# Kernel tuning notes

Measured on AMD Instinct MI355X. Metric: run time of the kernel, lower is better.

The kernel has to match this reference:

```python
import jax, jax.numpy as jnp
import numpy as np

N, E, D_IN, HID, HEADS, TS_OUT = 100000, 200000, 165, 64, 8, 5
HD1 = HID // HEADS  # 8 per-head channels in layer 1
HD2 = HID           # 64 per-head channels in layer 2 (concat=False -> mean)


def _glorot(key, shape):
    fan_in, fan_out = shape[0], shape[1]
    s = np.sqrt(6.0 / (fan_in + fan_out)).astype(np.float32)
    return jax.random.uniform(key, shape, jnp.float32, -s, s)


def setup_inputs() -> dict:
    key = jax.random.key(0)
    ks = jax.random.split(key, 24)
    inp = {
        "x": jax.random.normal(ks[0], (N, D_IN), jnp.float32),
        "edge_index": jax.random.randint(ks[1], (2, E), 0, N, jnp.int32),
        "timestamp_target": jax.random.randint(ks[2], (N,), 0, TS_OUT, jnp.int32),
        "node_target": jax.random.randint(ks[3], (N,), 0, 2, jnp.int32),
        "node_mask": jax.random.randint(ks[4], (N,), 0, 2, jnp.int32).astype(jnp.bool_),
        # GATConv layer 1: in=165 -> 8 heads x 8 ch, concat -> 64
        "W1": _glorot(ks[5], (D_IN, HEADS * HD1)),
        "att_src1": _glorot(ks[6], (HEADS, HD1)),
        "att_dst1": _glorot(ks[7], (HEADS, HD1)),
        "b1": jnp.zeros((HEADS * HD1,), jnp.float32),
        # GATConv layer 2: in=64 -> 8 heads x 64 ch, mean -> 64
        "W2": _glorot(ks[8], (HID, HEADS * HD2)),
        "att_src2": _glorot(ks[9], (HEADS, HD2)),
        "att_dst2": _glorot(ks[10], (HEADS, HD2)),
        "b2": jnp.zeros((HD2,), jnp.float32),
        # timestamp predictor MLP
        "ts_w1": _glorot(ks[11], (HID, HID)), "ts_b1": jnp.zeros((HID,), jnp.float32),
        "ts_w2": _glorot(ks[12], (HID, TS_OUT)), "ts_b2": jnp.zeros((TS_OUT,), jnp.float32),
        # class predictor MLP
        "cls_w1": _glorot(ks[13], (HID, HID)), "cls_b1": jnp.zeros((HID,), jnp.float32),
        "cls_w2": _glorot(ks[14], (HID, 2)), "cls_b2": jnp.zeros((2,), jnp.float32),
    }
    return inp


def _gat_layer(x, src, dst, n, W, a_src, a_dst, b, concat):
    H, C = a_src.shape
    h = (x @ W).reshape(n, H, C)                      # [N,H,C]
    a_s = (h * a_src).sum(-1)                         # [N,H]
    a_d = (h * a_dst).sum(-1)                         # [N,H]
    alpha = jax.nn.leaky_relu(a_s[src] + a_d[dst], 0.2)   # [E,H]
    amax = jax.ops.segment_max(alpha, dst, num_segments=n)
    ea = jnp.exp(alpha - amax[dst])
    denom = jax.ops.segment_sum(ea, dst, num_segments=n)
    a = ea / (denom[dst] + 1e-16)                     # segment softmax over incoming edges
    out = jax.ops.segment_sum(h[src] * a[:, :, None], dst, num_segments=n)  # [N,H,C]
    out = out.reshape(n, H * C) if concat else out.mean(axis=1)
    return out + b


def _ce(logits, targets):
    lp = jax.nn.log_softmax(logits, axis=-1)
    return -jnp.take_along_axis(lp, targets[:, None].astype(jnp.int32), axis=1)[:, 0]


def reference(x, edge_index, timestamp_target, node_target, node_mask,
              W1, att_src1, att_dst1, b1, W2, att_src2, att_dst2, b2,
              ts_w1, ts_b1, ts_w2, ts_b2, cls_w1, cls_b1, cls_w2, cls_b2):
    n = x.shape[0]
    loops = jnp.arange(n, dtype=edge_index.dtype)
    src = jnp.concatenate([edge_index[0], loops])     # add self loops (PyG default)
    dst = jnp.concatenate([edge_index[1], loops])
    h = _gat_layer(x, src, dst, n, W1, att_src1, att_dst1, b1, True)   # [N,64]
    h = _gat_layer(h, src, dst, n, W2, att_src2, att_dst2, b2, False)  # [N,64]
    # gradient reversal is identity in the forward pass
    ts_pred = jax.nn.relu(h @ ts_w1 + ts_b1) @ ts_w2 + ts_b2           # [N,5]
    cls_pred = jax.nn.relu(h @ cls_w1 + cls_b1) @ cls_w2 + cls_b2      # [N,2]
    ts_loss = _ce(ts_pred, timestamp_target).mean()
    m = node_mask.astype(jnp.float32)
    cls_loss = (_ce(cls_pred, node_target) * m).sum() / m.sum()
    return cls_loss + 1.0 * ts_loss
```

## Files before the change

kernel.cpp:

```cpp
#include <hip/hip_runtime.h>
#include <hip/hip_bf16.h>

#define NN 100000
#define NE 200000
#define NT (NE + NN)
#define DIN 165
#define CHUNK 50000
#define PREPB 128
#define INITB 391
#define PACKB 8
#define W1PB 24
#define MISCGRID (PREPB + INITB + PACKB + W1PB)
#define NODEB 1563
#define XDW ((size_t)NN * DIN)
#define NDMA 42

typedef __attribute__((ext_vector_type(8))) short bf16x8_t;
typedef __attribute__((ext_vector_type(4))) float f32x4_t;
typedef _Float16 h2_t __attribute__((ext_vector_type(2)));
typedef _Float16 f16x8_t __attribute__((ext_vector_type(8)));

#define AS1 __attribute__((address_space(1)))
#define AS3 __attribute__((address_space(3)))

static __device__ __forceinline__ unsigned short f2bf(float f) {
    __hip_bfloat16 b = __float2bfloat16(f);
    return *(unsigned short*)&b;
}
static __device__ __forceinline__ float bfu(unsigned short u) {
    __hip_bfloat16 b = *(__hip_bfloat16*)&u;
    return __bfloat162float(b);
}
static __device__ __forceinline__ unsigned pkh2(float a, float b) {
    h2_t v; v[0] = (_Float16)a; v[1] = (_Float16)b;
    return *(unsigned*)&v;
}


__global__ __launch_bounds__(256) void k_misc(const float* W2, const float* a2s, const float* a2d,
                                              float* wsd, __hip_bfloat16* W2pT,
                                              int* cnt, int* fill,
                                              const float* tsw1, const float* cw1,
                                              unsigned* tswp, unsigned* cwp,
                                              const float* W1, unsigned* W1pT, float* zbuf) {
    int b = blockIdx.x;
    int tid = threadIdx.x;
    if (b < PREPB) {
        int i = b * 256 + tid;
        int c = i >> 9, j = i & 511;
        int hh = j >> 6, kk = j & 63;
        W2pT[i] = __float2bfloat16(W2[kk * 512 + hh * 64 + c]);
        if (b == 0) zbuf[tid] = 0.f;
        if (i < 512) {
            int h = i >> 6, k = i & 63;
            float s = 0.f, d = 0.f;
            for (int cc = 0; cc < 64; cc++) {
                float w = W2[k * 512 + h * 64 + cc];
                s += w * a2s[h * 64 + cc];
                d += w * a2d[h * 64 + cc];
            }
            wsd[i] = s; wsd[512 + i] = d;
        }
    } else if (b < PREPB + INITB) {
        int i = (b - PREPB) * 256 + tid;
        if (i < NN) { cnt[i] = 0; fill[i] = 0; }
    } else if (b < PREPB + INITB + PACKB) {
        int i = (b - PREPB - INITB) * 256 + tid;
        if (i < 2048) {
            int kp = i >> 6, c = i & 63;
            tswp[i] = pkh2(tsw1[(2 * kp) * 64 + c], tsw1[(2 * kp + 1) * 64 + c]);
            cwp[i]  = pkh2(cw1[(2 * kp) * 64 + c],  cw1[(2 * kp + 1) * 64 + c]);
        }
    } else {
        int i = (b - PREPB - INITB - PACKB) * 256 + tid;
        if (i < 6144) {
            int c = i / 96, kp = i - c * 96;
            int k = 2 * kp;
            float f0 = (k < DIN) ? W1[k * 64 + c] : 0.f;
            float f1 = (k + 1 < DIN) ? W1[(k + 1) * 64 + c] : 0.f;
            W1pT[i] = pkh2(f0, f1);
        }
    }
}


__global__ __launch_bounds__(256) void k_count(const int* dstE, int* cnt) {
    int e = blockIdx.x * 256 + threadIdx.x;
    if (e < NE) atomicAdd(&cnt[dstE[e]], 1);
}

__global__ __launch_bounds__(256) void k_scanA(const int* cnt, int* rowptr, int* bsum) {
    __shared__ int sm[256];
    int t = threadIdx.x;
    int base = blockIdx.x * 1024;
    int v[4]; int s = 0;
    for (int i = 0; i < 4; i++) {
        int idx = base + t * 4 + i;
        v[i] = (idx < NN) ? (cnt[idx] + 1) : 0;
        s += v[i];
    }
    sm[t] = s; __syncthreads();
    for (int off = 1; off < 256; off <<= 1) {
        int x = (t >= off) ? sm[t - off] : 0;
        __syncthreads();
        sm[t] += x;
        __syncthreads();
    }
    int run = sm[t] - s;
    for (int i = 0; i < 4; i++) {
        run += v[i];
        int idx = base + t * 4 + i;
        if (idx < NN) rowptr[idx + 1] = run;
    }
    if (t == 255) bsum[blockIdx.x] = sm[255];
}

__global__ __launch_bounds__(64) void k_scanB(int* bsum, int nb) {
    int lane = threadIdx.x;
    int v0 = (lane < nb) ? bsum[lane] : 0;
    int v1 = (64 + lane < nb) ? bsum[64 + lane] : 0;
    int s0 = v0;
    for (int off = 1; off < 64; off <<= 1) { int t = __shfl_up(s0, off); if (lane >= off) s0 += t; }
    int tot0 = __shfl(s0, 63);
    int s1 = v1;
    for (int off = 1; off < 64; off <<= 1) { int t = __shfl_up(s1, off); if (lane >= off) s1 += t; }
    if (lane < nb) bsum[lane] = s0 - v0;
    if (64 + lane < nb) bsum[64 + lane] = tot0 + s1 - v1;
}

__global__ __launch_bounds__(256) void k_scanC(const int* bsum, int* rowptr) {
    int i = blockIdx.x * 256 + threadIdx.x;
    if (i < NN) rowptr[i + 1] += bsum[i >> 10];
    if (i == 0) rowptr[0] = 0;
}

__global__ __launch_bounds__(256) void k_fill(const int* srcE, const int* dstE,
                                              const int* rowptr, int* fill, int* col, int* rowv) {
    int i = blockIdx.x * 256 + threadIdx.x;
    if (i >= NT) return;
    int s, d;
    if (i < NE) { s = srcE[i]; d = dstE[i]; }
    else        { s = i - NE; d = s; }
    int p = rowptr[d] + atomicAdd(&fill[d], 1);
    col[p] = s;
    rowv[p] = d;
}


__global__ __launch_bounds__(256) void k_gemm1(const float* x, const unsigned* W1pT,
                                               const float* att_s, const float* att_d,
                                               const float* zsrc,
                                               __hip_bfloat16* h1b, float* aad1) {
    __shared__ float X[NDMA * 256];
    int tid = threadIdx.x;
    int l = tid & 63, w = tid >> 6;
    int n0 = blockIdx.x * 64;
    int frow = l & 15, kg = l >> 4;

    size_t tb = (size_t)n0 * DIN;
    for (int i = w; i < NDMA; i += 4) {
        size_t gd = tb + (size_t)i * 256 + (size_t)l * 4;
        const float* g = (gd + 4 <= XDW) ? (x + gd) : (zsrc + l * 4);
        __builtin_amdgcn_global_load_lds((const AS1 float*)g,
                                         (AS3 float*)(X + i * 256), 16, 0, 0);
    }
    uint4 B[6][4];
    #pragma unroll
    for (int s = 0; s < 6; s++)
        #pragma unroll
        for (int t = 0; t < 4; t++)
            B[s][t] = *(const uint4*)&W1pT[(t * 16 + frow) * 96 + s * 16 + kg * 4];
    __syncthreads();

    f32x4_t acc[4] = {};
    int rbase = (w * 16 + frow) * DIN + kg * 8;
    #pragma unroll
    for (int s = 0; s < 6; s++) {
        float f[8];
        #pragma unroll
        for (int j = 0; j < 8; j++) f[j] = X[rbase + s * 32 + j];
        f16x8_t av;
        #pragma unroll
        for (int j = 0; j < 8; j++) av[j] = (_Float16)f[j];
        #pragma unroll
        for (int t = 0; t < 4; t++)
            acc[t] = __builtin_amdgcn_mfma_f32_16x16x32_f16(av, *(f16x8_t*)&B[s][t], acc[t], 0, 0, 0);
    }

    int nw = n0 + w * 16;
    float asv[4], adv[4];
    #pragma unroll
    for (int t = 0; t < 4; t++) {
        int c = t * 16 + frow;
        asv[t] = att_s[c]; adv[t] = att_d[c];
    }
    int hb = (l >> 3) & 1;
    #pragma unroll
    for (int q = 0; q < 4; q++) {
        int n = nw + kg * 4 + q;
        bool ok = (n < NN);
        #pragma unroll
        for (int t = 0; t < 4; t++) {
            float sv = acc[t][q] * asv[t];
            float dv = acc[t][q] * adv[t];
            sv += __shfl_xor(sv, 1); sv += __shfl_xor(sv, 2); sv += __shfl_xor(sv, 4);
            dv += __shfl_xor(dv, 1); dv += __shfl_xor(dv, 2); dv += __shfl_xor(dv, 4);
            if (ok && (l & 7) == 0) {
                int h = t * 2 + hb;
                aad1[(size_t)n * 16 + h]     = sv;
                aad1[(size_t)n * 16 + 8 + h] = dv;
            }
        }
    }

    __syncthreads();
    unsigned short* Hw = (unsigned short*)X + w * 1152;
    #pragma unroll
    for (int t = 0; t < 4; t++)
        #pragma unroll
        for (int q = 0; q < 4; q++)
            Hw[(kg * 4 + q) * 72 + t * 16 + frow] = f2bf(acc[t][q]);
    int rr = l >> 2, cc = l & 3;
    int n2 = nw + rr;
    if (n2 < NN) {
        unsigned short* dst = (unsigned short*)h1b + (size_t)n2 * 64 + cc * 16;
        *(uint4*)dst       = *(const uint4*)&Hw[rr * 72 + cc * 16];
        *(uint4*)(dst + 8) = *(const uint4*)&Hw[rr * 72 + cc * 16 + 8];
    }
}


__global__ __launch_bounds__(256) void k_edgew(const float* aad, const int* col, const int* rowv,
                                               __hip_bfloat16* web) {
    int e = blockIdx.x * 256 + threadIdx.x;
    if (e >= NT) return;
    int s = col[e], d = rowv[e];
    float4 s0 = *(const float4*)&aad[(size_t)s * 16];
    float4 s1 = *(const float4*)&aad[(size_t)s * 16 + 4];
    float4 dd0 = *(const float4*)&aad[(size_t)d * 16 + 8];
    float4 dd1 = *(const float4*)&aad[(size_t)d * 16 + 12];
    float as[8] = {s0.x, s0.y, s0.z, s0.w, s1.x, s1.y, s1.z, s1.w};
    float ad[8] = {dd0.x, dd0.y, dd0.z, dd0.w, dd1.x, dd1.y, dd1.z, dd1.w};
    unsigned p[4];
    #pragma unroll
    for (int q = 0; q < 4; q++) {
        float a0 = as[2*q]   + ad[2*q];
        float a1 = as[2*q+1] + ad[2*q+1];
        a0 = a0 > 0.f ? a0 : 0.2f * a0;
        a1 = a1 > 0.f ? a1 : 0.2f * a1;
        p[q] = (unsigned)f2bf(__expf(a0)) | ((unsigned)f2bf(__expf(a1)) << 16);
    }
    *(uint4*)&web[(size_t)e * 8] = make_uint4(p[0], p[1], p[2], p[3]);
}


__global__ __launch_bounds__(256) void k_agg1(const __hip_bfloat16* h1b, const __hip_bfloat16* we1b,
                                              const int* rowptr, const int* col,
                                              const float* b1, __hip_bfloat16* out1b) {
    int tid = threadIdx.x;
    int q = tid & 15;
    int n = blockIdx.x * 16 + (tid >> 4);
    int hq = q >> 1;
    const unsigned short* h1u = (const unsigned short*)h1b;
    const unsigned short* weu = (const unsigned short*)we1b;
    int rs = rowptr[n], re = rowptr[n + 1];
    float acc0 = 0.f, acc1 = 0.f, acc2 = 0.f, acc3 = 0.f, den = 0.f;
    for (int eb = rs; eb < re; eb += 4) {
        int c4[4];
        #pragma unroll
        for (int j = 0; j < 4; j++) c4[j] = col[min(eb + j, re - 1)];
        #pragma unroll
        for (int j = 0; j < 4; j++) {
            int e = min(eb + j, re - 1);
            float wv = bfu(weu[(size_t)e * 8 + hq]);
            wv = (eb + j < re) ? wv : 0.f;
            uint2 hv = *(const uint2*)&h1u[(size_t)c4[j] * 64 + q * 4];
            den  += wv;
            acc0 += wv * bfu((unsigned short)(hv.x & 0xffff));
            acc1 += wv * bfu((unsigned short)(hv.x >> 16));
            acc2 += wv * bfu((unsigned short)(hv.y & 0xffff));
            acc3 += wv * bfu((unsigned short)(hv.y >> 16));
        }
    }
    float4 bb = *(const float4*)&b1[q * 4];
    float dd = den + 1e-16f;
    unsigned short* ou = (unsigned short*)out1b;
    unsigned p0 = (unsigned)f2bf(acc0 / dd + bb.x) | ((unsigned)f2bf(acc1 / dd + bb.y) << 16);
    unsigned p1 = (unsigned)f2bf(acc2 / dd + bb.z) | ((unsigned)f2bf(acc3 / dd + bb.w) << 16);
    *(uint2*)&ou[(size_t)n * 64 + q * 4] = make_uint2(p0, p1);
}


__global__ __launch_bounds__(256) void k_att2(const __hip_bfloat16* out1b, const float* wsd,
                                              float* aad2) {
    __shared__ float t[64][65];
    int tid = threadIdx.x;
    int n0 = blockIdx.x * 64;
    const unsigned short* o1u = (const unsigned short*)out1b;
    #pragma unroll
    for (int l = 0; l < 4; l++) {
        int q = tid + l * 256;
        int r = q >> 4, c4 = q & 15;
        int n = n0 + r;
        uint2 v = make_uint2(0, 0);
        if (n < NN) v = *(const uint2*)&o1u[(size_t)n * 64 + c4 * 4];
        t[r][c4 * 4 + 0] = bfu((unsigned short)(v.x & 0xffff));
        t[r][c4 * 4 + 1] = bfu((unsigned short)(v.x >> 16));
        t[r][c4 * 4 + 2] = bfu((unsigned short)(v.y & 0xffff));
        t[r][c4 * 4 + 3] = bfu((unsigned short)(v.y >> 16));
    }
    __syncthreads();
    int lane = tid & 63;
    int j0 = __builtin_amdgcn_readfirstlane((tid >> 6) * 4);
    int n = n0 + lane;
    float a0 = 0.f, a1 = 0.f, a2 = 0.f, a3 = 0.f;
    #pragma unroll 8
    for (int k = 0; k < 64; k++) {
        float ov = t[lane][k];
        a0 += ov * wsd[(j0 + 0) * 64 + k];
        a1 += ov * wsd[(j0 + 1) * 64 + k];
        a2 += ov * wsd[(j0 + 2) * 64 + k];
        a3 += ov * wsd[(j0 + 3) * 64 + k];
    }
    if (n < NN) *(float4*)&aad2[(size_t)n * 16 + j0] = make_float4(a0, a1, a2, a3);
}


__global__ __launch_bounds__(256) void k_agg2(const __hip_bfloat16* out1b, const __hip_bfloat16* we2b,
                                              const int* rowptr, const int* col,
                                              __hip_bfloat16* aggb, int n0, int n1) {
    int tid = threadIdx.x;
    int p = tid & 31;
    int n = n0 + blockIdx.x * 8 + (tid >> 5);
    const unsigned short* o1u = (const unsigned short*)out1b;
    const unsigned short* weu = (const unsigned short*)we2b;
    int rs = rowptr[n], re = rowptr[n + 1];
    float den[8] = {}, a0[8] = {}, a1[8] = {};
    for (int eb = rs; eb < re; eb += 4) {
        int c4[4];
        #pragma unroll
        for (int j = 0; j < 4; j++) c4[j] = col[min(eb + j, re - 1)];
        #pragma unroll
        for (int j = 0; j < 4; j++) {
            int e = min(eb + j, re - 1);
            uint4 wv = *(const uint4*)&weu[(size_t)e * 8];
            unsigned hv = *(const unsigned*)&o1u[(size_t)c4[j] * 64 + p * 2];
            float vmul = (eb + j < re) ? 1.f : 0.f;
            float h0 = bfu((unsigned short)(hv & 0xffff));
            float h1 = bfu((unsigned short)(hv >> 16));
            float wts[8] = {bfu((unsigned short)(wv.x & 0xffff)), bfu((unsigned short)(wv.x >> 16)),
                            bfu((unsigned short)(wv.y & 0xffff)), bfu((unsigned short)(wv.y >> 16)),
                            bfu((unsigned short)(wv.z & 0xffff)), bfu((unsigned short)(wv.z >> 16)),
                            bfu((unsigned short)(wv.w & 0xffff)), bfu((unsigned short)(wv.w >> 16))};
            #pragma unroll
            for (int hh = 0; hh < 8; hh++) {
                float ww = wts[hh] * vmul;
                den[hh] += ww;
                a0[hh] += ww * h0;
                a1[hh] += ww * h1;
            }
        }
    }
    size_t base = (size_t)(n - n0) * 512;
    unsigned short* au = (unsigned short*)aggb;
    #pragma unroll
    for (int hh = 0; hh < 8; hh++) {
        float dd = den[hh] + 1e-16f;
        unsigned pp = (unsigned)f2bf(a0[hh] / dd) | ((unsigned)f2bf(a1[hh] / dd) << 16);
        *(unsigned*)&au[base + hh * 64 + p * 2] = pp;
    }
}


__global__ __launch_bounds__(256) void k_gemm2(const __hip_bfloat16* aggb, const __hip_bfloat16* W2pT,
                                               const float* b2, __hip_bfloat16* out2Tb, int n0, int n1) {
    __shared__ float smem[4608];
    unsigned short* A_lds = (unsigned short*)smem;
    unsigned short* B_lds = A_lds + 64 * 72;
    const unsigned short* A_g = (const unsigned short*)aggb;
    const unsigned short* B_g = (const unsigned short*)W2pT;
    int tid = threadIdx.x;
    int w = tid >> 6, l = tid & 63;
    int m0 = blockIdx.x * 64;
    int rows = n1 - n0;
    f32x4_t acc[4] = {};
    for (int k0 = 0; k0 < 512; k0 += 64) {
        #pragma unroll
        for (int ll = 0; ll < 2; ll++) {
            int u = tid + ll * 256;
            int r = u >> 3, seg = u & 7;
            uint4 va = make_uint4(0, 0, 0, 0);
            if (m0 + r < rows) va = *(const uint4*)&A_g[(size_t)(m0 + r) * 512 + k0 + seg * 8];
            *(uint4*)&A_lds[r * 72 + seg * 8] = va;
            *(uint4*)&B_lds[r * 72 + seg * 8] = *(const uint4*)&B_g[(size_t)r * 512 + k0 + seg * 8];
        }
        __syncthreads();
        #pragma unroll
        for (int kk = 0; kk < 2; kk++) {
            bf16x8_t a = *(const bf16x8_t*)&A_lds[(w * 16 + (l & 15)) * 72 + kk * 32 + (l >> 4) * 8];
            #pragma unroll
            for (int t = 0; t < 4; t++) {
                bf16x8_t bb = *(const bf16x8_t*)&B_lds[(t * 16 + (l & 15)) * 72 + kk * 32 + (l >> 4) * 8];
                acc[t] = __builtin_amdgcn_mfma_f32_16x16x32_bf16(a, bb, acc[t], 0, 0, 0);
            }
        }
        __syncthreads();
    }
    #pragma unroll
    for (int t = 0; t < 4; t++) {
        int col_l = l & 15;
        float bias = b2[t * 16 + col_l];
        #pragma unroll
        for (int q = 0; q < 4; q++) {
            int row_l = (l >> 4) * 4 + q;
            smem[(w * 16 + row_l) * 66 + t * 16 + col_l] = 0.125f * acc[t][q] + bias;
        }
    }
    __syncthreads();
    unsigned short* o2u = (unsigned short*)out2Tb;
    int ml = tid & 63, cr = tid >> 6;
    #pragma unroll
    for (int p = 0; p < 16; p++) {
        int c = p * 4 + cr;
        int gr = m0 + ml;
        if (gr < rows) o2u[(size_t)c * NN + (n0 + gr)] = f2bf(smem[ml * 66 + c]);
    }
}


__global__ __launch_bounds__(256) void k_mlp(const __hip_bfloat16* out2Tb,
                                             const unsigned* tswp, const float* tsb1,
                                             const float* tsw2, const float* tsb2,
                                             const unsigned* cwp, const float* cb1,
                                             const float* cw2, const float* cb2,
                                             const int* tst, const int* ctg, const unsigned char* msk,
                                             float* part) {
    __shared__ unsigned t2h[32 * 64];
    __shared__ float red[4][7][64];
    int tid = threadIdx.x;
    int lane = tid & 63;
    int w = tid >> 6;
    int n0 = blockIdx.x * 64;
    int nstage = n0 + lane; if (nstage >= NN) nstage = NN - 1;
    const unsigned short* o2u = (const unsigned short*)out2Tb;
    #pragma unroll
    for (int l = 0; l < 8; l++) {
        int kp = w * 8 + l;
        float e0 = bfu(o2u[(size_t)(2 * kp) * NN + nstage]);
        float e1 = bfu(o2u[(size_t)(2 * kp + 1) * NN + nstage]);
        t2h[kp * 64 + lane] = pkh2(e0, e1);
    }
    __syncthreads();

    int c0 = __builtin_amdgcn_readfirstlane(w * 16);
    int n = n0 + lane;
    float vts[16], vcls[16];
    #pragma unroll
    for (int j = 0; j < 16; j++) { vts[j] = tsb1[c0 + j]; vcls[j] = cb1[c0 + j]; }
    for (int kp = 0; kp < 32; kp++) {
        unsigned ou = t2h[kp * 64 + lane];
        h2_t ov = *(h2_t*)&ou;
        const unsigned* wt = &tswp[kp * 64 + c0];
        const unsigned* wc = &cwp[kp * 64 + c0];
        #pragma unroll
        for (int j = 0; j < 16; j++) {
            unsigned wtv = wt[j], wcv = wc[j];
            vts[j]  = __builtin_amdgcn_fdot2(ov, *(h2_t*)&wtv, vts[j], false);
            vcls[j] = __builtin_amdgcn_fdot2(ov, *(h2_t*)&wcv, vcls[j], false);
        }
    }
    float lg[5] = {0.f, 0.f, 0.f, 0.f, 0.f};
    float lg2[2] = {0.f, 0.f};
    #pragma unroll
    for (int j = 0; j < 16; j++) {
        int c = c0 + j;
        float v = fmaxf(vts[j], 0.f);
        #pragma unroll
        for (int t = 0; t < 5; t++) lg[t] += v * tsw2[c * 5 + t];
        float v2 = fmaxf(vcls[j], 0.f);
        lg2[0] += v2 * cw2[c * 2];
        lg2[1] += v2 * cw2[c * 2 + 1];
    }
    #pragma unroll
    for (int t = 0; t < 5; t++) red[w][t][lane] = lg[t];
    red[w][5][lane] = lg2[0];
    red[w][6][lane] = lg2[1];
    __syncthreads();
    if (w == 0) {
        float tsl = 0.f, cll = 0.f, mval = 0.f;
        if (n < NN) {
            float L[5];
            #pragma unroll
            for (int t = 0; t < 5; t++)
                L[t] = red[0][t][lane] + red[1][t][lane] + red[2][t][lane] + red[3][t][lane] + tsb2[t];
            float mx = L[0];
            #pragma unroll
            for (int t = 1; t < 5; t++) mx = fmaxf(mx, L[t]);
            float se = 0.f;
            #pragma unroll
            for (int t = 0; t < 5; t++) se += __expf(L[t] - mx);
            int tg = tst[n];
            float pick = 0.f;
            #pragma unroll
            for (int t = 0; t < 5; t++) pick += (t == tg) ? L[t] : 0.f;
            tsl = mx + __logf(se) - pick;
            float C0 = red[0][5][lane] + red[1][5][lane] + red[2][5][lane] + red[3][5][lane] + cb2[0];
            float C1 = red[0][6][lane] + red[1][6][lane] + red[2][6][lane] + red[3][6][lane] + cb2[1];
            float mx2 = fmaxf(C0, C1);
            float lse2 = mx2 + __logf(__expf(C0 - mx2) + __expf(C1 - mx2));
            mval = msk[n] ? 1.f : 0.f;
            float pick2 = ctg[n] ? C1 : C0;
            cll = (lse2 - pick2) * mval;
        }
        #pragma unroll
        for (int off = 1; off < 64; off <<= 1) {
            tsl  += __shfl_xor(tsl, off);
            cll  += __shfl_xor(cll, off);
            mval += __shfl_xor(mval, off);
        }
        if (lane == 0) {
            part[blockIdx.x * 3 + 0] = tsl;
            part[blockIdx.x * 3 + 1] = cll;
            part[blockIdx.x * 3 + 2] = mval;
        }
    }
}

__global__ __launch_bounds__(256) void k_final(const float* part, float* out, int nb) {
    __shared__ float sm[3][256];
    int tid = threadIdx.x;
    float a = 0, b = 0, c = 0;
    for (int i = tid; i < nb; i += 256) { a += part[i*3]; b += part[i*3+1]; c += part[i*3+2]; }
    sm[0][tid] = a; sm[1][tid] = b; sm[2][tid] = c;
    __syncthreads();
    for (int s = 128; s > 0; s >>= 1) {
        if (tid < s) {
            sm[0][tid] += sm[0][tid + s];
            sm[1][tid] += sm[1][tid + s];
            sm[2][tid] += sm[2][tid + s];
        }
        __syncthreads();
    }
    if (tid == 0) out[0] = sm[1][0] / sm[2][0] + sm[0][0] / (float)NN;
}


extern "C" void kernel_launch(void* const* d_in, const int* in_sizes, int n_in,
                              void* d_out, int out_size, void* d_ws, size_t ws_size,
                              hipStream_t stream) {
    const float* x    = (const float*)d_in[0];
    const int*   ei   = (const int*)d_in[1];
    const int*   tst  = (const int*)d_in[2];
    const int*   ctg  = (const int*)d_in[3];
    const unsigned char* msk = (const unsigned char*)d_in[4];
    const float* W1   = (const float*)d_in[5];
    const float* a1s  = (const float*)d_in[6];
    const float* a1d  = (const float*)d_in[7];
    const float* b1   = (const float*)d_in[8];
    const float* W2   = (const float*)d_in[9];
    const float* a2s  = (const float*)d_in[10];
    const float* a2d  = (const float*)d_in[11];
    const float* b2   = (const float*)d_in[12];
    const float* tsw1 = (const float*)d_in[13];
    const float* tsb1 = (const float*)d_in[14];
    const float* tsw2 = (const float*)d_in[15];
    const float* tsb2 = (const float*)d_in[16];
    const float* cw1  = (const float*)d_in[17];
    const float* cb1  = (const float*)d_in[18];
    const float* cw2  = (const float*)d_in[19];
    const float* cb2  = (const float*)d_in[20];
    const int* srcE = ei;
    const int* dstE = ei + NE;

    char* ws = (char*)d_ws;
    size_t off = 0;
    auto alloc = [&](size_t b) { size_t o = off; off = (off + b + 255) & ~(size_t)255; return o; };
    int*   cnt    = (int*)(ws + alloc((size_t)NN * 4));
    int*   fill   = (int*)(ws + alloc((size_t)NN * 4));
    int*   rowptr = (int*)(ws + alloc((size_t)(NN + 1) * 4));
    int*   bsum   = (int*)(ws + alloc(128 * 4));
    int*   col    = (int*)(ws + alloc((size_t)NT * 4));
    int*   rowv   = (int*)(ws + alloc((size_t)NT * 4));
    float* aad1   = (float*)(ws + alloc((size_t)NN * 16 * 4));
    __hip_bfloat16* out1b = (__hip_bfloat16*)(ws + alloc((size_t)NN * 64 * 2));
    float* aad2   = (float*)(ws + alloc((size_t)NN * 16 * 4));
    float* wsd    = (float*)(ws + alloc(1024 * 4));
    __hip_bfloat16* W2pT  = (__hip_bfloat16*)(ws + alloc(32768 * 2));
    unsigned* tswp = (unsigned*)(ws + alloc(2048 * 4));
    unsigned* cwp  = (unsigned*)(ws + alloc(2048 * 4));
    unsigned* W1pT = (unsigned*)(ws + alloc(6144 * 4));
    float* zbuf   = (float*)(ws + alloc(256 * 4));
    __hip_bfloat16* out2Tb = (__hip_bfloat16*)(ws + alloc((size_t)NN * 64 * 2));
    __hip_bfloat16* h1b   = (__hip_bfloat16*)(ws + alloc((size_t)NN * 64 * 2));
    __hip_bfloat16* aggb  = (__hip_bfloat16*)(ws + alloc((size_t)CHUNK * 512 * 2));
    __hip_bfloat16* web   = (__hip_bfloat16*)(ws + alloc((size_t)NT * 8 * 2));
    float* part   = (float*)(ws + alloc((size_t)NODEB * 3 * 4));
    (void)ws_size; (void)in_sizes; (void)n_in; (void)out_size;

    int nb_scan = (NN + 1023) / 1024;

    k_misc<<<MISCGRID, 256, 0, stream>>>(W2, a2s, a2d, wsd, W2pT, cnt, fill,
                                         tsw1, cw1, tswp, cwp, W1, W1pT, zbuf);
    k_count<<<(NE + 255) / 256, 256, 0, stream>>>(dstE, cnt);
    k_scanA<<<nb_scan, 256, 0, stream>>>(cnt, rowptr, bsum);
    k_scanB<<<1, 64, 0, stream>>>(bsum, nb_scan);
    k_scanC<<<(NN + 255) / 256, 256, 0, stream>>>(bsum, rowptr);
    k_fill<<<(NT + 255) / 256, 256, 0, stream>>>(srcE, dstE, rowptr, fill, col, rowv);

    k_gemm1<<<NODEB, 256, 0, stream>>>(x, W1pT, a1s, a1d, zbuf, h1b, aad1);
    k_edgew<<<(NT + 255) / 256, 256, 0, stream>>>(aad1, col, rowv, web);
    k_agg1<<<NN / 16, 256, 0, stream>>>(h1b, web, rowptr, col, b1, out1b);
    k_att2<<<NODEB, 256, 0, stream>>>(out1b, wsd, aad2);
    k_edgew<<<(NT + 255) / 256, 256, 0, stream>>>(aad2, col, rowv, web);

    for (int c = 0; c < 2; c++) {
        int n0 = c * CHUNK, n1 = n0 + CHUNK;
        k_agg2<<<CHUNK / 8, 256, 0, stream>>>(out1b, web, rowptr, col, aggb, n0, n1);
        k_gemm2<<<(CHUNK + 63) / 64, 256, 0, stream>>>(aggb, W2pT, b2, out2Tb, n0, n1);
    }

    k_mlp<<<NODEB, 256, 0, stream>>>(out2Tb, tswp, tsb1, tsw2, tsb2,
                                     cwp, cb1, cw2, cb2, tst, ctg, msk, part);
    k_final<<<1, 256, 0, stream>>>(part, (float*)d_out, NODEB);
}
```

Measured before the change: 213.5 us.

## Fuse layer-2 aggregation, projection GEMM and MLP losses into one kernel

Replaces the chunked layer-2 aggregation, the GEMM over the aggregated 512-wide features and the separate MLP/loss kernel with one fused kernel. Per-node head-wise aggregates now stay in a swizzled LDS tile that feeds MFMA directly, and the MLP first layers also run on MFMA from LDS, so the large intermediate aggregate and transposed output buffers are never written to global memory. Separately, the first-layer GEMM moves to 32-row, 128-thread blocks and drops its bounds checks. The fused kernel uses about 73KB of LDS per block, which limits occupancy and may hurt latency hiding in the gather-heavy aggregation phase.

```diff
diff --git a/kernel.cpp b/kernel.cpp
--- a/kernel.cpp
+++ b/kernel.cpp
@@ -5,15 +5,15 @@
 #define NE 200000
 #define NT (NE + NN)
 #define DIN 165
-#define CHUNK 50000
 #define PREPB 128
 #define INITB 391
-#define PACKB 8
+#define PACKB 32
 #define W1PB 24
 #define MISCGRID (PREPB + INITB + PACKB + W1PB)
 #define NODEB 1563
 #define XDW ((size_t)NN * DIN)
-#define NDMA 42
+#define G1ROWS 32
+#define G1NDMA 21
 
 typedef __attribute__((ext_vector_type(8))) short bf16x8_t;
 typedef __attribute__((ext_vector_type(4))) float f32x4_t;
@@ -41,7 +41,7 @@
                                               float* wsd, __hip_bfloat16* W2pT,
                                               int* cnt, int* fill,
                                               const float* tsw1, const float* cw1,
-                                              unsigned* tswp, unsigned* cwp,
+                                              __hip_bfloat16* wB,
                                               const float* W1, unsigned* W1pT, float* zbuf) {
     int b = blockIdx.x;
     int tid = threadIdx.x;
@@ -66,10 +66,10 @@
         if (i < NN) { cnt[i] = 0; fill[i] = 0; }
     } else if (b < PREPB + INITB + PACKB) {
         int i = (b - PREPB - INITB) * 256 + tid;
-        if (i < 2048) {
-            int kp = i >> 6, c = i & 63;
-            tswp[i] = pkh2(tsw1[(2 * kp) * 64 + c], tsw1[(2 * kp + 1) * 64 + c]);
-            cwp[i]  = pkh2(cw1[(2 * kp) * 64 + c],  cw1[(2 * kp + 1) * 64 + c]);
+        if (i < 8192) {
+            int c = i >> 6, k = i & 63;
+            float v = (c < 64) ? tsw1[k * 64 + c] : cw1[k * 64 + (c - 64)];
+            wB[i] = __float2bfloat16(v);
         }
     } else {
         int i = (b - PREPB - INITB - PACKB) * 256 + tid;
@@ -147,18 +147,18 @@
 }
 
 
-__global__ __launch_bounds__(256) void k_gemm1(const float* x, const unsigned* W1pT,
+__global__ __launch_bounds__(128) void k_gemm1(const float* x, const unsigned* W1pT,
                                                const float* att_s, const float* att_d,
                                                const float* zsrc,
                                                __hip_bfloat16* h1b, float* aad1) {
-    __shared__ float X[NDMA * 256];
+    __shared__ float X[G1NDMA * 256];
     int tid = threadIdx.x;
     int l = tid & 63, w = tid >> 6;
-    int n0 = blockIdx.x * 64;
+    int n0 = blockIdx.x * G1ROWS;
     int frow = l & 15, kg = l >> 4;
 
     size_t tb = (size_t)n0 * DIN;
-    for (int i = w; i < NDMA; i += 4) {
+    for (int i = w; i < G1NDMA; i += 2) {
         size_t gd = tb + (size_t)i * 256 + (size_t)l * 4;
         const float* g = (gd + 4 <= XDW) ? (x + gd) : (zsrc + l * 4);
         __builtin_amdgcn_global_load_lds((const AS1 float*)g,
@@ -176,12 +176,9 @@
     int rbase = (w * 16 + frow) * DIN + kg * 8;
     #pragma unroll
     for (int s = 0; s < 6; s++) {
-        float f[8];
-        #pragma unroll
-        for (int j = 0; j < 8; j++) f[j] = X[rbase + s * 32 + j];
         f16x8_t av;
         #pragma unroll
-        for (int j = 0; j < 8; j++) av[j] = (_Float16)f[j];
+        for (int j = 0; j < 8; j++) av[j] = (_Float16)X[rbase + s * 32 + j];
         #pragma unroll
         for (int t = 0; t < 4; t++)
             acc[t] = __builtin_amdgcn_mfma_f32_16x16x32_f16(av, *(f16x8_t*)&B[s][t], acc[t], 0, 0, 0);
@@ -198,14 +195,13 @@
     #pragma unroll
     for (int q = 0; q < 4; q++) {
         int n = nw + kg * 4 + q;
-        bool ok = (n < NN);
         #pragma unroll
         for (int t = 0; t < 4; t++) {
             float sv = acc[t][q] * asv[t];
             float dv = acc[t][q] * adv[t];
             sv += __shfl_xor(sv, 1); sv += __shfl_xor(sv, 2); sv += __shfl_xor(sv, 4);
             dv += __shfl_xor(dv, 1); dv += __shfl_xor(dv, 2); dv += __shfl_xor(dv, 4);
-            if (ok && (l & 7) == 0) {
+            if ((l & 7) == 0) {
                 int h = t * 2 + hb;
                 aad1[(size_t)n * 16 + h]     = sv;
                 aad1[(size_t)n * 16 + 8 + h] = dv;
@@ -222,11 +218,9 @@
             Hw[(kg * 4 + q) * 72 + t * 16 + frow] = f2bf(acc[t][q]);
     int rr = l >> 2, cc = l & 3;
     int n2 = nw + rr;
-    if (n2 < NN) {
-        unsigned short* dst = (unsigned short*)h1b + (size_t)n2 * 64 + cc * 16;
-        *(uint4*)dst       = *(const uint4*)&Hw[rr * 72 + cc * 16];
-        *(uint4*)(dst + 8) = *(const uint4*)&Hw[rr * 72 + cc * 16 + 8];
-    }
+    unsigned short* dst = (unsigned short*)h1b + (size_t)n2 * 64 + cc * 16;
+    *(uint4*)dst       = *(const uint4*)&Hw[rr * 72 + cc * 16];
+    *(uint4*)(dst + 8) = *(const uint4*)&Hw[rr * 72 + cc * 16 + 8];
 }
 
 
@@ -326,203 +320,213 @@
 }
 
 
-__global__ __launch_bounds__(256) void k_agg2(const __hip_bfloat16* out1b, const __hip_bfloat16* we2b,
-                                              const int* rowptr, const int* col,
-                                              __hip_bfloat16* aggb, int n0, int n1) {
+__global__ __launch_bounds__(256) void k_l2f(const __hip_bfloat16* out1b, const __hip_bfloat16* we2b,
+                                             const int* rowptr, const int* col,
+                                             const __hip_bfloat16* W2pT, const float* b2,
+                                             const __hip_bfloat16* wB,
+                                             const float* tsb1, const float* cb1,
+                                             const float* tsw2, const float* tsb2,
+                                             const float* cw2, const float* cb2,
+                                             const int* tst, const int* ctg, const unsigned char* msk,
+                                             float* part) {
+    __shared__ unsigned short Ax[64 * 512];
+    __shared__ unsigned short Bl[64 * 72];
+    __shared__ float red[4][3];
     int tid = threadIdx.x;
-    int p = tid & 31;
-    int n = n0 + blockIdx.x * 8 + (tid >> 5);
+    int l = tid & 63, w = tid >> 6;
+    int n0 = blockIdx.x * 64;
+    int frow = l & 15, kg = l >> 4;
+
     const unsigned short* o1u = (const unsigned short*)out1b;
     const unsigned short* weu = (const unsigned short*)we2b;
-    int rs = rowptr[n], re = rowptr[n + 1];
-    float den[8] = {}, a0[8] = {}, a1[8] = {};
-    for (int eb = rs; eb < re; eb += 4) {
-        int c4[4];
-        #pragma unroll
-        for (int j = 0; j < 4; j++) c4[j] = col[min(eb + j, re - 1)];
-        #pragma unroll
-        for (int j = 0; j < 4; j++) {
-            int e = min(eb + j, re - 1);
-            uint4 wv = *(const uint4*)&weu[(size_t)e * 8];
-            unsigned hv = *(const unsigned*)&o1u[(size_t)c4[j] * 64 + p * 2];
-            float vmul = (eb + j < re) ? 1.f : 0.f;
-            float h0 = bfu((unsigned short)(hv & 0xffff));
-            float h1 = bfu((unsigned short)(hv >> 16));
-            float wts[8] = {bfu((unsigned short)(wv.x & 0xffff)), bfu((unsigned short)(wv.x >> 16)),
-                            bfu((unsigned short)(wv.y & 0xffff)), bfu((unsigned short)(wv.y >> 16)),
-                            bfu((unsigned short)(wv.z & 0xffff)), bfu((unsigned short)(wv.z >> 16)),
-                            bfu((unsigned short)(wv.w & 0xffff)), bfu((unsigned short)(wv.w >> 16))};
+    int q4 = tid & 15;
+    #pragma unroll 1
+    for (int pass = 0; pass < 4; pass++) {
+        int j = pass * 16 + (tid >> 4);
+        int n = n0 + j;
+        int rs = 0, re = 0;
+        if (n < NN) { rs = rowptr[n]; re = rowptr[n + 1]; }
+        float acc[8][4];
+        float den[8];
+        #pragma unroll
+        for (int h = 0; h < 8; h++) {
+            den[h] = 0.f;
             #pragma unroll
-            for (int hh = 0; hh < 8; hh++) {
-                float ww = wts[hh] * vmul;
-                den[hh] += ww;
-                a0[hh] += ww * h0;
-                a1[hh] += ww * h1;
+            for (int c = 0; c < 4; c++) acc[h][c] = 0.f;
+        }
+        for (int eb = rs; eb < re; eb += 4) {
+            int c4[4];
+            #pragma unroll
+            for (int jj = 0; jj < 4; jj++) c4[jj] = col[min(eb + jj, re - 1)];
+            #pragma unroll
+            for (int jj = 0; jj < 4; jj++) {
+                int e = min(eb + jj, re - 1);
+                uint4 wv = *(const uint4*)&weu[(size_t)e * 8];
+                uint2 hv = *(const uint2*)&o1u[(size_t)c4[jj] * 64 + q4 * 4];
+                float vm = (eb + jj < re) ? 1.f : 0.f;
+                float hc0 = bfu((unsigned short)(hv.x & 0xffff));
+                float hc1 = bfu((unsigned short)(hv.x >> 16));
+                float hc2 = bfu((unsigned short)(hv.y & 0xffff));
+                float hc3 = bfu((unsigned short)(hv.y >> 16));
+                float wt[8] = {bfu((unsigned short)(wv.x & 0xffff)), bfu((unsigned short)(wv.x >> 16)),
+                               bfu((unsigned short)(wv.y & 0xffff)), bfu((unsigned short)(wv.y >> 16)),
+                               bfu((unsigned short)(wv.z & 0xffff)), bfu((unsigned short)(wv.z >> 16)),
+                               bfu((unsigned short)(wv.w & 0xffff)), bfu((unsigned short)(wv.w >> 16))};
+                #pragma unroll
+                for (int h = 0; h < 8; h++) {
+                    float ww = wt[h] * vm;
+                    den[h] += ww;
+                    acc[h][0] += ww * hc0;
+                    acc[h][1] += ww * hc1;
+                    acc[h][2] += ww * hc2;
+                    acc[h][3] += ww * hc3;
+                }
             }
         }
-    }
-    size_t base = (size_t)(n - n0) * 512;
-    unsigned short* au = (unsigned short*)aggb;
-    #pragma unroll
-    for (int hh = 0; hh < 8; hh++) {
-        float dd = den[hh] + 1e-16f;
-        unsigned pp = (unsigned)f2bf(a0[hh] / dd) | ((unsigned)f2bf(a1[hh] / dd) << 16);
-        *(unsigned*)&au[base + hh * 64 + p * 2] = pp;
-    }
-}
-
-
-__global__ __launch_bounds__(256) void k_gemm2(const __hip_bfloat16* aggb, const __hip_bfloat16* W2pT,
-                                               const float* b2, __hip_bfloat16* out2Tb, int n0, int n1) {
-    __shared__ float smem[4608];
-    unsigned short* A_lds = (unsigned short*)smem;
-    unsigned short* B_lds = A_lds + 64 * 72;
-    const unsigned short* A_g = (const unsigned short*)aggb;
+        #pragma unroll
+        for (int h = 0; h < 8; h++) {
+            float dd = den[h] + 1e-16f;
+            unsigned lo = (unsigned)f2bf(acc[h][0] / dd) | ((unsigned)f2bf(acc[h][1] / dd) << 16);
+            unsigned hi = (unsigned)f2bf(acc[h][2] / dd) | ((unsigned)f2bf(acc[h][3] / dd) << 16);
+            int blk = (h * 8 + (q4 >> 1)) ^ (j & 7);
+            *(uint2*)&Ax[j * 512 + blk * 8 + (q4 & 1) * 4] = make_uint2(lo, hi);
+        }
+    }
+    __syncthreads();
+
     const unsigned short* B_g = (const unsigned short*)W2pT;
-    int tid = threadIdx.x;
-    int w = tid >> 6, l = tid & 63;
-    int m0 = blockIdx.x * 64;
-    int rows = n1 - n0;
-    f32x4_t acc[4] = {};
+    f32x4_t gacc[4] = {};
     for (int k0 = 0; k0 < 512; k0 += 64) {
         #pragma unroll
         for (int ll = 0; ll < 2; ll++) {
             int u = tid + ll * 256;
             int r = u >> 3, seg = u & 7;
-            uint4 va = make_uint4(0, 0, 0, 0);
-            if (m0 + r < rows) va = *(const uint4*)&A_g[(size_t)(m0 + r) * 512 + k0 + seg * 8];
-            *(uint4*)&A_lds[r * 72 + seg * 8] = va;
-            *(uint4*)&B_lds[r * 72 + seg * 8] = *(const uint4*)&B_g[(size_t)r * 512 + k0 + seg * 8];
+            *(uint4*)&Bl[r * 72 + seg * 8] = *(const uint4*)&B_g[(size_t)r * 512 + k0 + seg * 8];
         }
         __syncthreads();
         #pragma unroll
         for (int kk = 0; kk < 2; kk++) {
-            bf16x8_t a = *(const bf16x8_t*)&A_lds[(w * 16 + (l & 15)) * 72 + kk * 32 + (l >> 4) * 8];
+            int blk = ((k0 >> 3) + kk * 4 + kg) ^ (frow & 7);
+            bf16x8_t a = *(const bf16x8_t*)&Ax[(w * 16 + frow) * 512 + blk * 8];
             #pragma unroll
             for (int t = 0; t < 4; t++) {
-                bf16x8_t bb = *(const bf16x8_t*)&B_lds[(t * 16 + (l & 15)) * 72 + kk * 32 + (l >> 4) * 8];
-                acc[t] = __builtin_amdgcn_mfma_f32_16x16x32_bf16(a, bb, acc[t], 0, 0, 0);
+                bf16x8_t bb = *(const bf16x8_t*)&Bl[(t * 16 + frow) * 72 + kk * 32 + kg * 8];
+                gacc[t] = __builtin_amdgcn_mfma_f32_16x16x32_bf16(a, bb, gacc[t], 0, 0, 0);
             }
         }
         __syncthreads();
     }
+
+    unsigned short* o2L = Ax;
     #pragma unroll
     for (int t = 0; t < 4; t++) {
-        int col_l = l & 15;
-        float bias = b2[t * 16 + col_l];
+        float bias = b2[t * 16 + frow];
+        #pragma unroll
+        for (int q = 0; q < 4; q++)
+            o2L[(w * 16 + kg * 4 + q) * 72 + t * 16 + frow] = f2bf(0.125f * gacc[t][q] + bias);
+    }
+    __syncthreads();
+    const unsigned short* wBu = (const unsigned short*)wB;
+    f32x4_t a2c[8] = {};
+    #pragma unroll
+    for (int kk = 0; kk < 2; kk++) {
+        bf16x8_t a2 = *(const bf16x8_t*)&o2L[(w * 16 + frow) * 72 + kk * 32 + kg * 8];
+        #pragma unroll
+        for (int t2 = 0; t2 < 8; t2++) {
+            bf16x8_t b2f = *(const bf16x8_t*)&wBu[(t2 * 16 + frow) * 64 + kk * 32 + kg * 8];
+            a2c[t2] = __builtin_amdgcn_mfma_f32_16x16x32_bf16(a2, b2f, a2c[t2], 0, 0, 0);
+        }
+    }
+
+    float lg[4][5]; float lc[4][2];
+    #pragma unroll
+    for (int q = 0; q < 4; q++) {
+        #pragma unroll
+        for (int t = 0; t < 5; t++) lg[q][t] = 0.f;
+        lc[q][0] = 0.f; lc[q][1] = 0.f;
+    }
+    #pragma unroll
+    for (int t2 = 0; t2 < 4; t2++) {
+        int c = t2 * 16 + frow;
+        float bb = tsb1[c];
+        float w0 = tsw2[c * 5 + 0], w1 = tsw2[c * 5 + 1], w2 = tsw2[c * 5 + 2],
+              w3 = tsw2[c * 5 + 3], w4 = tsw2[c * 5 + 4];
         #pragma unroll
         for (int q = 0; q < 4; q++) {
-            int row_l = (l >> 4) * 4 + q;
-            smem[(w * 16 + row_l) * 66 + t * 16 + col_l] = 0.125f * acc[t][q] + bias;
-        }
-    }
+            float v = fmaxf(a2c[t2][q] + bb, 0.f);
+            lg[q][0] += v * w0; lg[q][1] += v * w1; lg[q][2] += v * w2;
+            lg[q][3] += v * w3; lg[q][4] += v * w4;
+        }
+    }
+    #pragma unroll
+    for (int t2 = 0; t2 < 4; t2++) {
+        int c = t2 * 16 + frow;
+        float bb = cb1[c];
+        float u0 = cw2[c * 2], u1 = cw2[c * 2 + 1];
+        #pragma unroll
+        for (int q = 0; q < 4; q++) {
+            float v = fmaxf(a2c[t2 + 4][q] + bb, 0.f);
+            lc[q][0] += v * u0; lc[q][1] += v * u1;
+        }
+    }
+    #pragma unroll
+    for (int q = 0; q < 4; q++) {
+        #pragma unroll
+        for (int t = 0; t < 5; t++) {
+            lg[q][t] += __shfl_xor(lg[q][t], 1);
+            lg[q][t] += __shfl_xor(lg[q][t], 2);
+            lg[q][t] += __shfl_xor(lg[q][t], 4);
+            lg[q][t] += __shfl_xor(lg[q][t], 8);
+        }
+        #pragma unroll
+        for (int t = 0; t < 2; t++) {
+            lc[q][t] += __shfl_xor(lc[q][t], 1);
+            lc[q][t] += __shfl_xor(lc[q][t], 2);
+            lc[q][t] += __shfl_xor(lc[q][t], 4);
+            lc[q][t] += __shfl_xor(lc[q][t], 8);
+        }
+    }
+    float tsl = 0.f, cll = 0.f, mval = 0.f;
+    if (frow == 0) {
+        #pragma unroll
+        for (int q = 0; q < 4; q++) {
+            int n = n0 + w * 16 + kg * 4 + q;
+            if (n < NN) {
+                float L[5];
+                #pragma unroll
+                for (int t = 0; t < 5; t++) L[t] = lg[q][t] + tsb2[t];
+                float mx = fmaxf(fmaxf(fmaxf(L[0], L[1]), fmaxf(L[2], L[3])), L[4]);
+                float se = 0.f;
+                #pragma unroll
+                for (int t = 0; t < 5; t++) se += __expf(L[t] - mx);
+                int tg = tst[n];
+                float pick = 0.f;
+                #pragma unroll
+                for (int t = 0; t < 5; t++) pick += (t == tg) ? L[t] : 0.f;
+                tsl += mx + __logf(se) - pick;
+                float C0 = lc[q][0] + cb2[0];
+                float C1 = lc[q][1] + cb2[1];
+                float mx2 = fmaxf(C0, C1);
+                float lse2 = mx2 + __logf(__expf(C0 - mx2) + __expf(C1 - mx2));
+                float mv = msk[n] ? 1.f : 0.f;
+                float pick2 = ctg[n] ? C1 : C0;
+                cll += (lse2 - pick2) * mv;
+                mval += mv;
+            }
+        }
+    }
+    #pragma unroll
+    for (int off = 1; off < 64; off <<= 1) {
+        tsl  += __shfl_xor(tsl, off);
+        cll  += __shfl_xor(cll, off);
+        mval += __shfl_xor(mval, off);
+    }
+    if (l == 0) { red[w][0] = tsl; red[w][1] = cll; red[w][2] = mval; }
     __syncthreads();
-    unsigned short* o2u = (unsigned short*)out2Tb;
-    int ml = tid & 63, cr = tid >> 6;
-    #pragma unroll
-    for (int p = 0; p < 16; p++) {
-        int c = p * 4 + cr;
-        int gr = m0 + ml;
-        if (gr < rows) o2u[(size_t)c * NN + (n0 + gr)] = f2bf(smem[ml * 66 + c]);
-    }
-}
-
-
-__global__ __launch_bounds__(256) void k_mlp(const __hip_bfloat16* out2Tb,
-                                             const unsigned* tswp, const float* tsb1,
-                                             const float* tsw2, const float* tsb2,
-                                             const unsigned* cwp, const float* cb1,
-                                             const float* cw2, const float* cb2,
-                                             const int* tst, const int* ctg, const unsigned char* msk,
-                                             float* part) {
-    __shared__ unsigned t2h[32 * 64];
-    __shared__ float red[4][7][64];
-    int tid = threadIdx.x;
-    int lane = tid & 63;
-    int w = tid >> 6;
-    int n0 = blockIdx.x * 64;
-    int nstage = n0 + lane; if (nstage >= NN) nstage = NN - 1;
-    const unsigned short* o2u = (const unsigned short*)out2Tb;
-    #pragma unroll
-    for (int l = 0; l < 8; l++) {
-        int kp = w * 8 + l;
-        float e0 = bfu(o2u[(size_t)(2 * kp) * NN + nstage]);
-        float e1 = bfu(o2u[(size_t)(2 * kp + 1) * NN + nstage]);
-        t2h[kp * 64 + lane] = pkh2(e0, e1);
-    }
-    __syncthreads();
-
-    int c0 = __builtin_amdgcn_readfirstlane(w * 16);
-    int n = n0 + lane;
-    float vts[16], vcls[16];
-    #pragma unroll
-    for (int j = 0; j < 16; j++) { vts[j] = tsb1[c0 + j]; vcls[j] = cb1[c0 + j]; }
-    for (int kp = 0; kp < 32; kp++) {
-        unsigned ou = t2h[kp * 64 + lane];
-        h2_t ov = *(h2_t*)&ou;
-        const unsigned* wt = &tswp[kp * 64 + c0];
-        const unsigned* wc = &cwp[kp * 64 + c0];
-        #pragma unroll
-        for (int j = 0; j < 16; j++) {
-            unsigned wtv = wt[j], wcv = wc[j];
-            vts[j]  = __builtin_amdgcn_fdot2(ov, *(h2_t*)&wtv, vts[j], false);
-            vcls[j] = __builtin_amdgcn_fdot2(ov, *(h2_t*)&wcv, vcls[j], false);
-        }
-    }
-    float lg[5] = {0.f, 0.f, 0.f, 0.f, 0.f};
-    float lg2[2] = {0.f, 0.f};
-    #pragma unroll
-    for (int j = 0; j < 16; j++) {
-        int c = c0 + j;
-        float v = fmaxf(vts[j], 0.f);
-        #pragma unroll
-        for (int t = 0; t < 5; t++) lg[t] += v * tsw2[c * 5 + t];
-        float v2 = fmaxf(vcls[j], 0.f);
-        lg2[0] += v2 * cw2[c * 2];
-        lg2[1] += v2 * cw2[c * 2 + 1];
-    }
-    #pragma unroll
-    for (int t = 0; t < 5; t++) red[w][t][lane] = lg[t];
-    red[w][5][lane] = lg2[0];
-    red[w][6][lane] = lg2[1];
-    __syncthreads();
-    if (w == 0) {
-        float tsl = 0.f, cll = 0.f, mval = 0.f;
-        if (n < NN) {
-            float L[5];
-            #pragma unroll
-            for (int t = 0; t < 5; t++)
-                L[t] = red[0][t][lane] + red[1][t][lane] + red[2][t][lane] + red[3][t][lane] + tsb2[t];
-            float mx = L[0];
-            #pragma unroll
-            for (int t = 1; t < 5; t++) mx = fmaxf(mx, L[t]);
-            float se = 0.f;
-            #pragma unroll
-            for (int t = 0; t < 5; t++) se += __expf(L[t] - mx);
-            int tg = tst[n];
-            float pick = 0.f;
-            #pragma unroll
-            for (int t = 0; t < 5; t++) pick += (t == tg) ? L[t] : 0.f;
-            tsl = mx + __logf(se) - pick;
-            float C0 = red[0][5][lane] + red[1][5][lane] + red[2][5][lane] + red[3][5][lane] + cb2[0];
-            float C1 = red[0][6][lane] + red[1][6][lane] + red[2][6][lane] + red[3][6][lane] + cb2[1];
-            float mx2 = fmaxf(C0, C1);
-            float lse2 = mx2 + __logf(__expf(C0 - mx2) + __expf(C1 - mx2));
-            mval = msk[n] ? 1.f : 0.f;
-            float pick2 = ctg[n] ? C1 : C0;
-            cll = (lse2 - pick2) * mval;
-        }
-        #pragma unroll
-        for (int off = 1; off < 64; off <<= 1) {
-            tsl  += __shfl_xor(tsl, off);
-            cll  += __shfl_xor(cll, off);
-            mval += __shfl_xor(mval, off);
-        }
-        if (lane == 0) {
-            part[blockIdx.x * 3 + 0] = tsl;
-            part[blockIdx.x * 3 + 1] = cll;
-            part[blockIdx.x * 3 + 2] = mval;
-        }
+    if (tid == 0) {
+        part[blockIdx.x * 3 + 0] = red[0][0] + red[1][0] + red[2][0] + red[3][0];
+        part[blockIdx.x * 3 + 1] = red[0][1] + red[1][1] + red[2][1] + red[3][1];
+        part[blockIdx.x * 3 + 2] = red[0][2] + red[1][2] + red[2][2] + red[3][2];
     }
 }
 
@@ -586,13 +590,10 @@
     float* aad2   = (float*)(ws + alloc((size_t)NN * 16 * 4));
     float* wsd    = (float*)(ws + alloc(1024 * 4));
     __hip_bfloat16* W2pT  = (__hip_bfloat16*)(ws + alloc(32768 * 2));
-    unsigned* tswp = (unsigned*)(ws + alloc(2048 * 4));
-    unsigned* cwp  = (unsigned*)(ws + alloc(2048 * 4));
+    __hip_bfloat16* wB    = (__hip_bfloat16*)(ws + alloc(8192 * 2));
     unsigned* W1pT = (unsigned*)(ws + alloc(6144 * 4));
     float* zbuf   = (float*)(ws + alloc(256 * 4));
-    __hip_bfloat16* out2Tb = (__hip_bfloat16*)(ws + alloc((size_t)NN * 64 * 2));
     __hip_bfloat16* h1b   = (__hip_bfloat16*)(ws + alloc((size_t)NN * 64 * 2));
-    __hip_bfloat16* aggb  = (__hip_bfloat16*)(ws + alloc((size_t)CHUNK * 512 * 2));
     __hip_bfloat16* web   = (__hip_bfloat16*)(ws + alloc((size_t)NT * 8 * 2));
     float* part   = (float*)(ws + alloc((size_t)NODEB * 3 * 4));
     (void)ws_size; (void)in_sizes; (void)n_in; (void)out_size;
@@ -600,26 +601,21 @@
     int nb_scan = (NN + 1023) / 1024;
 
     k_misc<<<MISCGRID, 256, 0, stream>>>(W2, a2s, a2d, wsd, W2pT, cnt, fill,
-                                         tsw1, cw1, tswp, cwp, W1, W1pT, zbuf);
+                                         tsw1, cw1, wB, W1, W1pT, zbuf);
     k_count<<<(NE + 255) / 256, 256, 0, stream>>>(dstE, cnt);
     k_scanA<<<nb_scan, 256, 0, stream>>>(cnt, rowptr, bsum);
     k_scanB<<<1, 64, 0, stream>>>(bsum, nb_scan);
     k_scanC<<<(NN + 255) / 256, 256, 0, stream>>>(bsum, rowptr);
     k_fill<<<(NT + 255) / 256, 256, 0, stream>>>(srcE, dstE, rowptr, fill, col, rowv);
 
-    k_gemm1<<<NODEB, 256, 0, stream>>>(x, W1pT, a1s, a1d, zbuf, h1b, aad1);
+    k_gemm1<<<NN / G1ROWS, 128, 0, stream>>>(x, W1pT, a1s, a1d, zbuf, h1b, aad1);
     k_edgew<<<(NT + 255) / 256, 256, 0, stream>>>(aad1, col, rowv, web);
     k_agg1<<<NN / 16, 256, 0, stream>>>(h1b, web, rowptr, col, b1, out1b);
     k_att2<<<NODEB, 256, 0, stream>>>(out1b, wsd, aad2);
     k_edgew<<<(NT + 255) / 256, 256, 0, stream>>>(aad2, col, rowv, web);
 
-    for (int c = 0; c < 2; c++) {
-        int n0 = c * CHUNK, n1 = n0 + CHUNK;
-        k_agg2<<<CHUNK / 8, 256, 0, stream>>>(out1b, web, rowptr, col, aggb, n0, n1);
-        k_gemm2<<<(CHUNK + 63) / 64, 256, 0, stream>>>(aggb, W2pT, b2, out2Tb, n0, n1);
-    }
-
-    k_mlp<<<NODEB, 256, 0, stream>>>(out2Tb, tswp, tsb1, tsw2, tsb2,
-                                     cwp, cb1, cw2, cb2, tst, ctg, msk, part);
+    k_l2f<<<NODEB, 256, 0, stream>>>(out1b, web, rowptr, col, W2pT, b2, wB,
+                                     tsb1, cb1, tsw2, tsb2, cw2, cb2, tst, ctg, msk, part);
+
     k_final<<<1, 256, 0, stream>>>(part, (float*)d_out, NODEB);
 }
```

Result: faster. 196.2 us (-8.1%).
